# Performance work log

Hardware: AMD Instinct MI355X
Metric: run time of the kernel (lower is better)

Reference implementation:

```python
import jax, jax.numpy as jnp
import numpy as np

B, C, L = 32, 128, 4096          # batch, n_channels, signal length
P, Q = 100, 20                   # n_projections, n_quantiles


def setup_inputs() -> dict:
    key = jax.random.key(0)
    k1, k2, k3, k4 = jax.random.split(key, 4)
    X = jax.random.normal(k1, (B, C, L), dtype=jnp.float32)
    # conv1d kernel of shape (P, C, 1) collapsed to (P, C)
    W = jax.random.normal(k2, (P, C), dtype=jnp.float32)
    s = 2.33 * jnp.sqrt(jnp.float32(C))
    min_vals = -s + 0.1 * jax.random.normal(k3, (P,), dtype=jnp.float32)
    max_vals = s + 0.1 * jax.random.normal(k4, (P,), dtype=jnp.float32)
    return {"X": X, "W": W, "min_vals": min_vals, "max_vals": max_vals}


def reference(X, W, min_vals, max_vals):
    # kernel-size-1 conv1d == channel projection
    a = jnp.einsum('bcl,pc->bpl', X, W)  # [B, P, L]
    fracs = jnp.arange(1, Q + 1, dtype=a.dtype) / jnp.asarray(Q + 1, a.dtype)
    thr = min_vals[None, :] + (max_vals - min_vals)[None, :] * fracs[:, None]  # [Q, P]

    def body(carry, t):  # t: [P] thresholds for one quantile
        cdf_q = jnp.mean((a < t[None, :, None]).astype(a.dtype), axis=-1)  # [B, P]
        return carry, cdf_q

    _, cdf = jax.lax.scan(body, None, thr)          # [Q, B, P]
    cdf = jnp.transpose(cdf, (1, 2, 0))             # [B, P, Q]
    return cdf.reshape(B, P * Q)
```

## Files before the change

### kernel.cpp

```cpp
#include <hip/hip_runtime.h>
#include <hip/hip_bf16.h>

#define B_   32
#define C_   128
#define L_   4096
#define P_   100
#define NPT  7
#define Q_   20
#define NBIN 21
#define NCH  (NPT * 4)
#define CHS  512

typedef short          bf16x8 __attribute__((ext_vector_type(8)));
typedef float          f32x4  __attribute__((ext_vector_type(4)));
typedef unsigned short u16x8  __attribute__((ext_vector_type(8)));

__device__ inline unsigned short f2bf(float f) {
    __hip_bfloat16 h = __float2bfloat16(f);
    unsigned short u; __builtin_memcpy(&u, &h, 2);
    return u;
}

__global__ void prep_w_kernel(const float* __restrict__ W, unsigned short* __restrict__ Wf) {
    const int t = blockIdx.x * 256 + threadIdx.x;
    if (t >= NCH * 64) return;
    const int chunk = t >> 6, lane = t & 63;
    const int pt = chunk >> 2, ks = chunk & 3;
    const int p  = pt * 16 + (lane & 15);
    const int c0 = ks * 32 + (lane >> 4) * 8;
    u16x8 v;
#pragma unroll
    for (int j = 0; j < 8; ++j)
        v[j] = (p < P_) ? f2bf(W[p * C_ + c0 + j]) : (unsigned short)0;
    *(u16x8*)(Wf + (size_t)t * 8) = v;
}

__global__ __launch_bounds__(256, 4)
void radon_mfma3_kernel(const float* __restrict__ X, const unsigned short* __restrict__ Wf,
                        const float* __restrict__ minv, const float* __restrict__ maxv,
                        float* __restrict__ out) {
    __shared__ unsigned short Wlds[NCH * CHS];
    __shared__ int   hist[P_ * NBIN];
    __shared__ float mn_s[P_], invd_s[P_];

    const int tid  = threadIdx.x;
    const int b    = blockIdx.y;
    const int lblk = blockIdx.x;
    const int wave = tid >> 6;
    const int lane = tid & 63;
    const int quad = lane >> 4;
    const int nn   = lane & 15;

    {
        const int4* src = (const int4*)Wf;
        int4* dst = (int4*)Wlds;
#pragma unroll
        for (int k = 0; k < NCH * 64 / 256; ++k)
            dst[tid + k * 256] = src[tid + k * 256];
    }
    for (int i = tid; i < P_; i += 256) {
        const float mn = minv[i];
        mn_s[i]   = mn;
        invd_s[i] = (float)NBIN / (maxv[i] - mn);
    }
    for (int i = tid; i < P_ * NBIN; i += 256) hist[i] = 0;
    __syncthreads();

    const int l0 = lblk * 128 + wave * 32;
    const float* Xb = X + (size_t)b * C_ * L_;
    float xv[2][4][8];
#pragma unroll
    for (int lt = 0; lt < 2; ++lt)
#pragma unroll
        for (int ks = 0; ks < 4; ++ks)
#pragma unroll
            for (int j = 0; j < 8; ++j)
                xv[lt][ks][j] = Xb[(size_t)(ks * 32 + quad * 8 + j) * L_ + l0 + lt * 16 + nn];

    bf16x8 bfrag[2][4];
#pragma unroll
    for (int lt = 0; lt < 2; ++lt)
#pragma unroll
        for (int ks = 0; ks < 4; ++ks) {
            unsigned int u[4];
#pragma unroll
            for (int jp = 0; jp < 4; ++jp) {
                __hip_bfloat162 h2 = __float22bfloat162_rn(
                    make_float2(xv[lt][ks][2 * jp], xv[lt][ks][2 * jp + 1]));
                __builtin_memcpy(&u[jp], &h2, 4);
            }
            __builtin_memcpy(&bfrag[lt][ks], u, 16);
        }

    for (int pt = 0; pt < NPT; ++pt) {
        bf16x8 afrag[4];
#pragma unroll
        for (int ks = 0; ks < 4; ++ks)
            afrag[ks] = *(const bf16x8*)(&Wlds[((pt * 4 + ks) * 64 + lane) * 8]);

        f32x4 acc0 = {0.f, 0.f, 0.f, 0.f};
        f32x4 acc1 = {0.f, 0.f, 0.f, 0.f};
#pragma unroll
        for (int ks = 0; ks < 4; ++ks) {
            acc0 = __builtin_amdgcn_mfma_f32_16x16x32_bf16(afrag[ks], bfrag[0][ks], acc0, 0, 0, 0);
            acc1 = __builtin_amdgcn_mfma_f32_16x16x32_bf16(afrag[ks], bfrag[1][ks], acc1, 0, 0, 0);
        }

#pragma unroll
        for (int r = 0; r < 4; ++r) {
            const int p = pt * 16 + quad * 4 + r;
            if (p < P_) {
                const float mn = mn_s[p], invd = invd_s[p];
                {
                    const float t = (acc0[r] - mn) * invd;
                    int k = 0;
                    if (t > 0.f) { const int ki = (int)t; k = (ki > 20) ? 20 : ki; }
                    atomicAdd(&hist[p * NBIN + k], 1);
                }
                {
                    const float t = (acc1[r] - mn) * invd;
                    int k = 0;
                    if (t > 0.f) { const int ki = (int)t; k = (ki > 20) ? 20 : ki; }
                    atomicAdd(&hist[p * NBIN + k], 1);
                }
            }
        }
    }
    __syncthreads();

    for (int i = tid; i < P_ * Q_; i += 256) {
        const int p  = i / Q_;
        const int qi = i - p * Q_;
        int s = 0;
        for (int k = 0; k <= qi; ++k) s += hist[p * NBIN + k];
        atomicAdd(&out[((size_t)b * P_ + p) * Q_ + qi], (float)s * (1.0f / (float)L_));
    }
}

extern "C" void kernel_launch(void* const* d_in, const int* in_sizes, int n_in,
                              void* d_out, int out_size, void* d_ws, size_t ws_size,
                              hipStream_t stream) {
    const float* X  = (const float*)d_in[0];
    const float* W  = (const float*)d_in[1];
    const float* mn = (const float*)d_in[2];
    const float* mx = (const float*)d_in[3];
    float* out = (float*)d_out;
    unsigned short* Wf = (unsigned short*)d_ws;

    hipMemsetAsync(out, 0, (size_t)out_size * sizeof(float), stream);
    prep_w_kernel<<<NCH * 64 / 256, 256, 0, stream>>>(W, Wf);

    dim3 grid(L_ / 128, B_);
    radon_mfma3_kernel<<<grid, dim3(256), 0, stream>>>(X, Wf, mn, mx, out);
}
```

Before: 109.2 us.

## Swap MFMA operand roles and process the two L-tiles in sequential passes

Result: slower. 136.5 us (+25.0%).

```diff
diff --git a/kernel.cpp b/kernel.cpp
--- a/kernel.cpp
+++ b/kernel.cpp
@@ -21,6 +21,17 @@
     return u;
 }
 
+__device__ inline bf16x8 pack8(const float* v) {
+    unsigned int u[4];
+#pragma unroll
+    for (int jp = 0; jp < 4; ++jp) {
+        __hip_bfloat162 h2 = __float22bfloat162_rn(make_float2(v[2 * jp], v[2 * jp + 1]));
+        __builtin_memcpy(&u[jp], &h2, 4);
+    }
+    bf16x8 r; __builtin_memcpy(&r, u, 16);
+    return r;
+}
+
 __global__ void prep_w_kernel(const float* __restrict__ W, unsigned short* __restrict__ Wf) {
     const int t = blockIdx.x * 256 + threadIdx.x;
     if (t >= NCH * 64) return;
@@ -36,7 +47,7 @@
 }
 
 __global__ __launch_bounds__(256, 4)
-void radon_mfma3_kernel(const float* __restrict__ X, const unsigned short* __restrict__ Wf,
+void radon_mfma4_kernel(const float* __restrict__ X, const unsigned short* __restrict__ Wf,
                         const float* __restrict__ minv, const float* __restrict__ maxv,
                         float* __restrict__ out) {
     __shared__ unsigned short Wlds[NCH * CHS];
@@ -67,65 +78,55 @@
     __syncthreads();
 
     const int l0 = lblk * 128 + wave * 32;
-    const float* Xb = X + (size_t)b * C_ * L_;
-    float xv[2][4][8];
+    const float* Xb = X + (size_t)b * C_ * L_ + l0 + nn;
+    float xv0[4][8], xv1[4][8];
 #pragma unroll
-    for (int lt = 0; lt < 2; ++lt)
+    for (int ks = 0; ks < 4; ++ks)
 #pragma unroll
-        for (int ks = 0; ks < 4; ++ks)
+        for (int j = 0; j < 8; ++j)
+            xv0[ks][j] = Xb[(size_t)(ks * 32 + quad * 8 + j) * L_];
 #pragma unroll
-            for (int j = 0; j < 8; ++j)
-                xv[lt][ks][j] = Xb[(size_t)(ks * 32 + quad * 8 + j) * L_ + l0 + lt * 16 + nn];
+    for (int ks = 0; ks < 4; ++ks)
+#pragma unroll
+        for (int j = 0; j < 8; ++j)
+            xv1[ks][j] = Xb[(size_t)(ks * 32 + quad * 8 + j) * L_ + 16];
 
-    bf16x8 bfrag[2][4];
-#pragma unroll
-    for (int lt = 0; lt < 2; ++lt)
-#pragma unroll
-        for (int ks = 0; ks < 4; ++ks) {
-            unsigned int u[4];
-#pragma unroll
-            for (int jp = 0; jp < 4; ++jp) {
-                __hip_bfloat162 h2 = __float22bfloat162_rn(
-                    make_float2(xv[lt][ks][2 * jp], xv[lt][ks][2 * jp + 1]));
-                __builtin_memcpy(&u[jp], &h2, 4);
-            }
-            __builtin_memcpy(&bfrag[lt][ks], u, 16);
-        }
-
-    for (int pt = 0; pt < NPT; ++pt) {
-        bf16x8 afrag[4];
-#pragma unroll
-        for (int ks = 0; ks < 4; ++ks)
-            afrag[ks] = *(const bf16x8*)(&Wlds[((pt * 4 + ks) * 64 + lane) * 8]);
-
-        f32x4 acc0 = {0.f, 0.f, 0.f, 0.f};
-        f32x4 acc1 = {0.f, 0.f, 0.f, 0.f};
-#pragma unroll
-        for (int ks = 0; ks < 4; ++ks) {
-            acc0 = __builtin_amdgcn_mfma_f32_16x16x32_bf16(afrag[ks], bfrag[0][ks], acc0, 0, 0, 0);
-            acc1 = __builtin_amdgcn_mfma_f32_16x16x32_bf16(afrag[ks], bfrag[1][ks], acc1, 0, 0, 0);
-        }
-
-#pragma unroll
-        for (int r = 0; r < 4; ++r) {
-            const int p = pt * 16 + quad * 4 + r;
+    auto run_pass = [&](const bf16x8* bfr) {
+#pragma unroll 2
+        for (int pt = 0; pt < NPT; ++pt) {
+            bf16x8 a0 = *(const bf16x8*)(&Wlds[((pt * 4 + 0) * 64 + lane) * 8]);
+            bf16x8 a1 = *(const bf16x8*)(&Wlds[((pt * 4 + 1) * 64 + lane) * 8]);
+            bf16x8 a2 = *(const bf16x8*)(&Wlds[((pt * 4 + 2) * 64 + lane) * 8]);
+            bf16x8 a3 = *(const bf16x8*)(&Wlds[((pt * 4 + 3) * 64 + lane) * 8]);
+            f32x4 acc = {0.f, 0.f, 0.f, 0.f};
+            acc = __builtin_amdgcn_mfma_f32_16x16x32_bf16(bfr[0], a0, acc, 0, 0, 0);
+            acc = __builtin_amdgcn_mfma_f32_16x16x32_bf16(bfr[1], a1, acc, 0, 0, 0);
+            acc = __builtin_amdgcn_mfma_f32_16x16x32_bf16(bfr[2], a2, acc, 0, 0, 0);
+            acc = __builtin_amdgcn_mfma_f32_16x16x32_bf16(bfr[3], a3, acc, 0, 0, 0);
+            const int p = pt * 16 + nn;
             if (p < P_) {
                 const float mn = mn_s[p], invd = invd_s[p];
-                {
-                    const float t = (acc0[r] - mn) * invd;
-                    int k = 0;
-                    if (t > 0.f) { const int ki = (int)t; k = (ki > 20) ? 20 : ki; }
-                    atomicAdd(&hist[p * NBIN + k], 1);
-                }
-                {
-                    const float t = (acc1[r] - mn) * invd;
+#pragma unroll
+                for (int r = 0; r < 4; ++r) {
+                    const float t = (acc[r] - mn) * invd;
                     int k = 0;
                     if (t > 0.f) { const int ki = (int)t; k = (ki > 20) ? 20 : ki; }
                     atomicAdd(&hist[p * NBIN + k], 1);
                 }
             }
         }
-    }
+    };
+
+    bf16x8 bfrag0[4];
+#pragma unroll
+    for (int ks = 0; ks < 4; ++ks) bfrag0[ks] = pack8(xv0[ks]);
+    run_pass(bfrag0);
+
+    bf16x8 bfrag1[4];
+#pragma unroll
+    for (int ks = 0; ks < 4; ++ks) bfrag1[ks] = pack8(xv1[ks]);
+    run_pass(bfrag1);
+
     __syncthreads();
 
     for (int i = tid; i < P_ * Q_; i += 256) {
@@ -151,5 +152,5 @@
     prep_w_kernel<<<NCH * 64 / 256, 256, 0, stream>>>(W, Wf);
 
     dim3 grid(L_ / 128, B_);
-    radon_mfma3_kernel<<<grid, dim3(256), 0, stream>>>(X, Wf, mn, mx, out);
+    radon_mfma4_kernel<<<grid, dim3(256), 0, stream>>>(X, Wf, mn, mx, out);
 }
```

## Use 1024-thread blocks over 512-sample spans and transpose MFMA operands for histogramming

Applied to the files above, without the earlier changes.

Measured after the change: 104.9 us. 1.04x faster.

```diff
diff --git a/kernel.cpp b/kernel.cpp
--- a/kernel.cpp
+++ b/kernel.cpp
@@ -1,15 +1,17 @@
 #include <hip/hip_runtime.h>
 #include <hip/hip_bf16.h>
 
-#define B_   32
-#define C_   128
-#define L_   4096
-#define P_   100
-#define NPT  7
-#define Q_   20
-#define NBIN 21
-#define NCH  (NPT * 4)
-#define CHS  512
+#define B_    32
+#define C_    128
+#define L_    4096
+#define P_    100
+#define NPT   7
+#define Q_    20
+#define NBIN  21
+#define NCH   (NPT * 4)
+#define CHS   512
+#define TPB   1024
+#define LSPAN 512
 
 typedef short          bf16x8 __attribute__((ext_vector_type(8)));
 typedef float          f32x4  __attribute__((ext_vector_type(4)));
@@ -35,8 +37,8 @@
     *(u16x8*)(Wf + (size_t)t * 8) = v;
 }
 
-__global__ __launch_bounds__(256, 4)
-void radon_mfma3_kernel(const float* __restrict__ X, const unsigned short* __restrict__ Wf,
+__global__ __launch_bounds__(TPB, 4)
+void radon_mfma5_kernel(const float* __restrict__ X, const unsigned short* __restrict__ Wf,
                         const float* __restrict__ minv, const float* __restrict__ maxv,
                         float* __restrict__ out) {
     __shared__ unsigned short Wlds[NCH * CHS];
@@ -54,19 +56,18 @@
     {
         const int4* src = (const int4*)Wf;
         int4* dst = (int4*)Wlds;
-#pragma unroll
-        for (int k = 0; k < NCH * 64 / 256; ++k)
-            dst[tid + k * 256] = src[tid + k * 256];
+        for (int k = tid; k < NCH * 64; k += TPB)
+            dst[k] = src[k];
     }
-    for (int i = tid; i < P_; i += 256) {
+    for (int i = tid; i < P_; i += TPB) {
         const float mn = minv[i];
         mn_s[i]   = mn;
         invd_s[i] = (float)NBIN / (maxv[i] - mn);
     }
-    for (int i = tid; i < P_ * NBIN; i += 256) hist[i] = 0;
+    for (int i = tid; i < P_ * NBIN; i += TPB) hist[i] = 0;
     __syncthreads();
 
-    const int l0 = lblk * 128 + wave * 32;
+    const int l0 = lblk * LSPAN + wave * 32;
     const float* Xb = X + (size_t)b * C_ * L_;
     float xv[2][4][8];
 #pragma unroll
@@ -102,33 +103,34 @@
         f32x4 acc1 = {0.f, 0.f, 0.f, 0.f};
 #pragma unroll
         for (int ks = 0; ks < 4; ++ks) {
-            acc0 = __builtin_amdgcn_mfma_f32_16x16x32_bf16(afrag[ks], bfrag[0][ks], acc0, 0, 0, 0);
-            acc1 = __builtin_amdgcn_mfma_f32_16x16x32_bf16(afrag[ks], bfrag[1][ks], acc1, 0, 0, 0);
+            acc0 = __builtin_amdgcn_mfma_f32_16x16x32_bf16(bfrag[0][ks], afrag[ks], acc0, 0, 0, 0);
+            acc1 = __builtin_amdgcn_mfma_f32_16x16x32_bf16(bfrag[1][ks], afrag[ks], acc1, 0, 0, 0);
         }
 
+        const int p = pt * 16 + nn;
+        if (p < P_) {
+            const float mn = mn_s[p], invd = invd_s[p];
+            int* __restrict__ hrow = &hist[p * NBIN];
 #pragma unroll
-        for (int r = 0; r < 4; ++r) {
-            const int p = pt * 16 + quad * 4 + r;
-            if (p < P_) {
-                const float mn = mn_s[p], invd = invd_s[p];
+            for (int r = 0; r < 4; ++r) {
                 {
                     const float t = (acc0[r] - mn) * invd;
                     int k = 0;
                     if (t > 0.f) { const int ki = (int)t; k = (ki > 20) ? 20 : ki; }
-                    atomicAdd(&hist[p * NBIN + k], 1);
+                    atomicAdd(&hrow[k], 1);
                 }
                 {
                     const float t = (acc1[r] - mn) * invd;
                     int k = 0;
                     if (t > 0.f) { const int ki = (int)t; k = (ki > 20) ? 20 : ki; }
-                    atomicAdd(&hist[p * NBIN + k], 1);
+                    atomicAdd(&hrow[k], 1);
                 }
             }
         }
     }
     __syncthreads();
 
-    for (int i = tid; i < P_ * Q_; i += 256) {
+    for (int i = tid; i < P_ * Q_; i += TPB) {
         const int p  = i / Q_;
         const int qi = i - p * Q_;
         int s = 0;
@@ -150,6 +152,6 @@
     hipMemsetAsync(out, 0, (size_t)out_size * sizeof(float), stream);
     prep_w_kernel<<<NCH * 64 / 256, 256, 0, stream>>>(W, Wf);
 
-    dim3 grid(L_ / 128, B_);
-    radon_mfma3_kernel<<<grid, dim3(256), 0, stream>>>(X, Wf, mn, mx, out);
+    dim3 grid(L_ / LSPAN, B_);
+    radon_mfma5_kernel<<<grid, dim3(TPB), 0, stream>>>(X, Wf, mn, mx, out);
 }
```
